# Performance work log

Hardware: AMD Instinct MI355X
Metric: run time of the kernel (lower is better)

## Reference

```python
import jax, jax.numpy as jnp
import numpy as np

N_ITEMS = 100000
H = 256
L = 3
B = 512


def setup_inputs() -> dict:
    key = jax.random.key(0)
    ks = jax.random.split(key, 9)
    s = 1.0 / np.sqrt(H)  # PyTorch GRU/Linear default uniform bound
    return {
        "input": jax.random.randint(ks[0], (B,), 0, N_ITEMS),
        "hidden": jnp.zeros((L, B, H), jnp.float32),
        "W_ih0": jax.random.uniform(ks[1], (3 * H, N_ITEMS), jnp.float32, -s, s),
        "W_ih_hi": jax.random.uniform(ks[2], (L - 1, 3 * H, H), jnp.float32, -s, s),
        "W_hh": jax.random.uniform(ks[3], (L, 3 * H, H), jnp.float32, -s, s),
        "b_ih": jax.random.uniform(ks[4], (L, 3 * H), jnp.float32, -s, s),
        "b_hh": jax.random.uniform(ks[5], (L, 3 * H), jnp.float32, -s, s),
        "W_out": jax.random.uniform(ks[6], (N_ITEMS, H), jnp.float32, -s, s),
        "b_out": jax.random.uniform(ks[7], (N_ITEMS,), jnp.float32, -s, s),
    }


def _gru_cell(x_proj, h, W_hh_l, b_hh_l):
    # PyTorch GRU cell; x_proj already holds x @ W_ih.T + b_ih
    h_proj = h @ W_hh_l.T + b_hh_l
    xr, xz, xn = jnp.split(x_proj, 3, axis=-1)
    hr, hz, hn = jnp.split(h_proj, 3, axis=-1)
    r = jax.nn.sigmoid(xr + hr)
    z = jax.nn.sigmoid(xz + hz)
    n = jnp.tanh(xn + r * hn)
    return (1.0 - z) * n + z * h


def reference(input, hidden, W_ih0, W_ih_hi, W_hh, b_ih, b_hh, W_out, b_out):
    # one_hot(input) @ W_ih0.T == row-gather of W_ih0.T  (same math, no dense one-hot)
    x_proj = W_ih0.T[input] + b_ih[0]  # (B, 3H)
    x = _gru_cell(x_proj, hidden[0], W_hh[0], b_hh[0])
    new_h = [x]
    for l in range(1, L):  # fixed small layer loop
        x_proj = x @ W_ih_hi[l - 1].T + b_ih[l]
        x = _gru_cell(x_proj, hidden[l], W_hh[l], b_hh[l])
        new_h.append(x)
    h_new = jnp.stack(new_h)  # (L, B, H)
    activation = jnp.tanh(x @ W_out.T + b_out)  # (B, N_ITEMS)
    return activation, h_new
```

## Files before the change

### kernel.cpp

```cpp
#include <hip/hip_runtime.h>
#include <math.h>
#include <stdint.h>

#define NI 100000
#define NB 512
#define NH 256
#define H3 768

typedef _Float16 f16x8 __attribute__((ext_vector_type(8)));
typedef float    f32x4 __attribute__((ext_vector_type(4)));

#define RAW_LDS_BARRIER() do {                                   \
    asm volatile("s_waitcnt lgkmcnt(0)" ::: "memory");           \
    __builtin_amdgcn_sched_barrier(0);                           \
    __builtin_amdgcn_s_barrier();                                \
    __builtin_amdgcn_sched_barrier(0);                           \
} while (0)

__device__ __forceinline__ float tanh_fast(float x) {
    x = fminf(fmaxf(x, -9.0f), 9.0f);
    const float e = __expf(2.0f * x);
    return (e - 1.0f) * __builtin_amdgcn_rcpf(e + 1.0f);
}
__device__ __forceinline__ float sigmoid_fast(float x) {
    return 1.0f / (1.0f + __expf(-x));
}

__global__ void k_gates0(const int* __restrict__ idx,
                         const float* __restrict__ Wih0,
                         const float* __restrict__ bih0,
                         const float* __restrict__ hp,
                         const float* __restrict__ hprev,
                         float* __restrict__ hnew)
{
    const int b = blockIdx.x;
    const int j = threadIdx.x;
    const int ib = idx[b];
    const float xr = Wih0[(size_t)(j          ) * NI + ib] + bih0[j];
    const float xz = Wih0[(size_t)(j + NH     ) * NI + ib] + bih0[j + NH];
    const float xn = Wih0[(size_t)(j + 2 * NH ) * NI + ib] + bih0[j + 2 * NH];
    const float hr = hp[b * H3 + j];
    const float hz = hp[b * H3 + NH + j];
    const float hn = hp[b * H3 + 2 * NH + j];
    const float h  = hprev[b * NH + j];
    const float r = sigmoid_fast(xr + hr);
    const float z = sigmoid_fast(xz + hz);
    const float n = tanh_fast(xn + r * hn);
    hnew[b * NH + j] = (1.0f - z) * n + z * h;
}

__global__ void k_gates(const float* __restrict__ xp,
                        const float* __restrict__ hp,
                        const float* __restrict__ hprev,
                        float* __restrict__ hnew)
{
    const int b = blockIdx.x;
    const int j = threadIdx.x;
    const float xr = xp[b * H3 + j];
    const float xz = xp[b * H3 + NH + j];
    const float xn = xp[b * H3 + 2 * NH + j];
    const float hr = hp[b * H3 + j];
    const float hz = hp[b * H3 + NH + j];
    const float hn = hp[b * H3 + 2 * NH + j];
    const float h  = hprev[b * NH + j];
    const float r = sigmoid_fast(xr + hr);
    const float z = sigmoid_fast(xz + hz);
    const float n = tanh_fast(xn + r * hn);
    hnew[b * NH + j] = (1.0f - z) * n + z * h;
}

__global__ void k_gates_last(const float* __restrict__ xp,
                             const float* __restrict__ hp,
                             const float* __restrict__ hprev,
                             float* __restrict__ hnew,
                             _Float16* __restrict__ Xh)
{
    const int b = blockIdx.x;
    const int j = threadIdx.x;
    const float xr = xp[b * H3 + j];
    const float xz = xp[b * H3 + NH + j];
    const float xn = xp[b * H3 + 2 * NH + j];
    const float hr = hp[b * H3 + j];
    const float hz = hp[b * H3 + NH + j];
    const float hn = hp[b * H3 + 2 * NH + j];
    const float h  = hprev[b * NH + j];
    const float r = sigmoid_fast(xr + hr);
    const float z = sigmoid_fast(xz + hz);
    const float n = tanh_fast(xn + r * hn);
    const float v = (1.0f - z) * n + z * h;
    hnew[b * NH + j] = v;
    Xh[b * NH + j] = (_Float16)v;
}

__global__ __launch_bounds__(256)
void k_gemm_small(const float* __restrict__ A0,
                  const float* __restrict__ B0,
                  const float* __restrict__ bias0,
                  float* __restrict__ C0,
                  int M, int N, int K,
                  int sA, int sB, int sBias, int sC)
{
    constexpr int BM = 64, BN = 64, BK = 64;
    __shared__ float As[BK][BM];
    __shared__ float Bs[BK][BN];

    const float* A    = A0 + (size_t)blockIdx.z * sA;
    const float* Bm   = B0 + (size_t)blockIdx.z * sB;
    const float* bias = bias0 + (size_t)blockIdx.z * sBias;
    float*       C    = C0 + (size_t)blockIdx.z * sC;

    const int tid = threadIdx.x;
    const int tx  = tid & 15;
    const int ty  = tid >> 4;
    const int m0  = blockIdx.x * BM;
    const int n0  = blockIdx.y * BN;

    float acc[4][4];
#pragma unroll
    for (int i = 0; i < 4; i++)
#pragma unroll
        for (int j = 0; j < 4; j++) acc[i][j] = 0.0f;

    for (int k0 = 0; k0 < K; k0 += BK) {
#pragma unroll
        for (int f = 0; f < 4; f++) {
            const int fid = tid + f * 256;
            const int row = fid >> 4;
            const int t4  = fid & 15;
            const int mp  = row ^ ((t4 & 3) << 3);
            {
                const float4 v = *(const float4*)(A + (size_t)(m0 + row) * K + k0 + t4 * 4);
                As[t4 * 4 + 0][mp] = v.x; As[t4 * 4 + 1][mp] = v.y;
                As[t4 * 4 + 2][mp] = v.z; As[t4 * 4 + 3][mp] = v.w;
            }
            {
                const float4 v = *(const float4*)(Bm + (size_t)(n0 + row) * K + k0 + t4 * 4);
                Bs[t4 * 4 + 0][mp] = v.x; Bs[t4 * 4 + 1][mp] = v.y;
                Bs[t4 * 4 + 2][mp] = v.z; Bs[t4 * 4 + 3][mp] = v.w;
            }
        }
        __syncthreads();
#pragma unroll
        for (int kk = 0; kk < BK; kk++) {
            const int s = ((kk >> 2) & 3) << 3;
            const float4 a0 = *(const float4*)&As[kk][(ty * 4) ^ s];
            const float4 b0 = *(const float4*)&Bs[kk][(tx * 4) ^ s];
            const float av[4] = {a0.x, a0.y, a0.z, a0.w};
            const float bv[4] = {b0.x, b0.y, b0.z, b0.w};
#pragma unroll
            for (int i = 0; i < 4; i++)
#pragma unroll
                for (int j = 0; j < 4; j++)
                    acc[i][j] = fmaf(av[i], bv[j], acc[i][j]);
        }
        __syncthreads();
    }

#pragma unroll
    for (int i = 0; i < 4; i++) {
        const size_t rowoff = (size_t)(m0 + ty * 4 + i) * N;
        const int gn = n0 + tx * 4;
        const float4 bb = *(const float4*)(bias + gn);
        float4 v;
        v.x = acc[i][0] + bb.x; v.y = acc[i][1] + bb.y;
        v.z = acc[i][2] + bb.z; v.w = acc[i][3] + bb.w;
        *(float4*)(C + rowoff + gn) = v;
    }
}

__global__ __launch_bounds__(512, 4)
void k_out_mfma(const _Float16* __restrict__ Xh,
                const float* __restrict__ W,
                const float* __restrict__ bout,
                float* __restrict__ C)
{
    __shared__ __align__(16) float S[16384];

    const int n0   = blockIdx.x * 64;
    const int tid  = threadIdx.x;
    const int w    = tid >> 6;
    const int lane = tid & 63;
    const int lr   = lane & 15;
    const int lg   = lane >> 4;

#pragma unroll
    for (int it = 0; it < 8; ++it) {
        const int fid = it * 512 + tid;
        const int row = fid >> 6;
        const int p   = fid & 63;
        int gr = n0 + row; if (gr >= NI) gr = NI - 1;
        const float* src = W + (size_t)gr * NH + (size_t)(p ^ (row & 7)) * 4;
        __builtin_amdgcn_global_load_lds(
            (const __attribute__((address_space(1))) void*)src,
            (__attribute__((address_space(3))) void*)(S + fid * 4),
            16, 0, 0);
    }

    f32x4 acc[4][4];
#pragma unroll
    for (int nf = 0; nf < 4; ++nf)
#pragma unroll
        for (int mf = 0; mf < 4; ++mf) acc[nf][mf] = (f32x4){0.f, 0.f, 0.f, 0.f};

    __syncthreads();

    const _Float16* xbase = Xh + (size_t)(w * 64 + lr) * NH + lg * 8;

#pragma unroll
    for (int t = 0; t < 8; ++t) {
        f16x8 xf[4];
#pragma unroll
        for (int mf = 0; mf < 4; ++mf)
            xf[mf] = *(const f16x8*)(xbase + mf * 16 * NH + t * 32);
#pragma unroll
        for (int nf = 0; nf < 4; ++nf) {
            const int rl = nf * 16 + lr;
            const int c0 = t * 8 + ((lg * 2)     ^ (rl & 7));
            const int c1 = t * 8 + ((lg * 2 + 1) ^ (rl & 7));
            const f32x4 u0 = *(const f32x4*)(S + rl * 256 + c0 * 4);
            const f32x4 u1 = *(const f32x4*)(S + rl * 256 + c1 * 4);
            f16x8 h;
            h[0] = (_Float16)u0[0]; h[1] = (_Float16)u0[1];
            h[2] = (_Float16)u0[2]; h[3] = (_Float16)u0[3];
            h[4] = (_Float16)u1[0]; h[5] = (_Float16)u1[1];
            h[6] = (_Float16)u1[2]; h[7] = (_Float16)u1[3];
#pragma unroll
            for (int mf = 0; mf < 4; ++mf)
                acc[nf][mf] = __builtin_amdgcn_mfma_f32_16x16x32_f16(
                    h, xf[mf], acc[nf][mf], 0, 0, 0);
        }
    }

#pragma unroll
    for (int pass = 0; pass < 2; ++pass) {
        RAW_LDS_BARRIER();
        if ((w >> 2) == pass) {
            const int mloc = (w & 3) * 64;
#pragma unroll
            for (int nf = 0; nf < 4; ++nf) {
                const int gn = n0 + nf * 16 + lg * 4;
                const float4 bb = (gn < NI) ? *(const float4*)(bout + gn)
                                            : make_float4(0.f, 0.f, 0.f, 0.f);
#pragma unroll
                for (int mf = 0; mf < 4; ++mf) {
                    const int mr = mloc + mf * 16 + lr;
                    const int p  = (nf * 4 + lg) ^ (lr & 7);
                    float4 v;
                    v.x = tanh_fast(acc[nf][mf][0] + bb.x);
                    v.y = tanh_fast(acc[nf][mf][1] + bb.y);
                    v.z = tanh_fast(acc[nf][mf][2] + bb.z);
                    v.w = tanh_fast(acc[nf][mf][3] + bb.w);
                    *(float4*)(S + mr * 64 + p * 4) = v;
                }
            }
        }
        RAW_LDS_BARRIER();
#pragma unroll
        for (int it = 0; it < 8; ++it) {
            const int fid = it * 512 + tid;
            const int row = fid >> 4;
            const int c   = fid & 15;
            const int gn  = n0 + c * 4;
            if (gn < NI) {
                const f32x4 v = *(const f32x4*)(S + row * 64 + ((c ^ (row & 7)) * 4));
                __builtin_nontemporal_store(
                    v, (f32x4*)(C + (size_t)(pass * 256 + row) * NI + gn));
            }
        }
    }
}

extern "C" void kernel_launch(void* const* d_in, const int* in_sizes, int n_in,
                              void* d_out, int out_size, void* d_ws, size_t ws_size,
                              hipStream_t stream)
{
    const int*   idx    = (const int*)  d_in[0];
    const float* hidden = (const float*)d_in[1];
    const float* Wih0   = (const float*)d_in[2];
    const float* WihHi  = (const float*)d_in[3];
    const float* Whh    = (const float*)d_in[4];
    const float* bih    = (const float*)d_in[5];
    const float* bhh    = (const float*)d_in[6];
    const float* Wout   = (const float*)d_in[7];
    const float* bout   = (const float*)d_in[8];

    float* act  = (float*)d_out;
    float* hnew = act + (size_t)NB * NI;
    float* hp = act;
    float* xp = act + 3 * NB * H3;
    _Float16* Xh = (_Float16*)d_ws;

    const dim3 bs(256);
    const dim3 gs_hp(NB / 64, H3 / 64, 3);
    const dim3 gs_xp(NB / 64, H3 / 64, 1);

    k_gemm_small<<<gs_hp, bs, 0, stream>>>(hidden, Whh, bhh, hp,
                                           NB, H3, NH, NB * NH, H3 * NH, H3, NB * H3);
    k_gates0<<<NB, bs, 0, stream>>>(idx, Wih0, bih, hp, hidden, hnew);
    k_gemm_small<<<gs_xp, bs, 0, stream>>>(hnew, WihHi, bih + H3, xp,
                                           NB, H3, NH, 0, 0, 0, 0);
    k_gates<<<NB, bs, 0, stream>>>(xp, hp + NB * H3, hidden + NB * NH, hnew + NB * NH);
    k_gemm_small<<<gs_xp, bs, 0, stream>>>(hnew + NB * NH, WihHi + H3 * NH, bih + 2 * H3, xp,
                                           NB, H3, NH, 0, 0, 0, 0);
    k_gates_last<<<NB, bs, 0, stream>>>(xp, hp + 2 * NB * H3, hidden + 2 * NB * NH,
                                        hnew + 2 * NB * NH, Xh);

    k_out_mfma<<<dim3((NI + 63) / 64), dim3(512), 0, stream>>>(Xh, Wout, bout, act);
}
```

Measured before the change: 147.3 us.

## Retile output GEMM to 128x256 blocks with double-buffered K-slice staging

The output projection kernel now tiles 128 item columns by 256 batch rows per block, with a 2x4 wave grid, instead of 64 columns by all 512 rows. W_out is staged into LDS in four 64-wide K slices, double-buffered so the next slice loads while MFMAs consume the current one. This is meant to overlap global loads with compute and cut the LDS footprint per stage. In exchange, each W_out tile is now loaded by two blocks (one per batch half), which doubles weight reads, and the loop adds extra barriers. The grid is hardcoded to 1564 blocks.

```diff
diff --git a/kernel.cpp b/kernel.cpp
--- a/kernel.cpp
+++ b/kernel.cpp
@@ -176,25 +176,33 @@
 {
     __shared__ __align__(16) float S[16384];
 
-    const int n0   = blockIdx.x * 64;
+    const int bid = blockIdx.x;
+    const int n0  = (bid >> 1) * 128;
+    const int m0  = (bid & 1) * 256;
+
     const int tid  = threadIdx.x;
     const int w    = tid >> 6;
     const int lane = tid & 63;
     const int lr   = lane & 15;
     const int lg   = lane >> 4;
-
-#pragma unroll
-    for (int it = 0; it < 8; ++it) {
-        const int fid = it * 512 + tid;
-        const int row = fid >> 6;
-        const int p   = fid & 63;
-        int gr = n0 + row; if (gr >= NI) gr = NI - 1;
-        const float* src = W + (size_t)gr * NH + (size_t)(p ^ (row & 7)) * 4;
-        __builtin_amdgcn_global_load_lds(
-            (const __attribute__((address_space(1))) void*)src,
-            (__attribute__((address_space(3))) void*)(S + fid * 4),
-            16, 0, 0);
-    }
+    const int wn   = w & 1;
+    const int wm   = w >> 1;
+
+    auto stage_q = [&](int q) {
+        float* buf = S + (q & 1) * 8192;
+#pragma unroll
+        for (int it = 0; it < 4; ++it) {
+            const int fid = it * 512 + tid;
+            const int row = fid >> 4;
+            const int p   = fid & 15;
+            int gr = n0 + row; if (gr >= NI) gr = NI - 1;
+            const float* src = W + (size_t)gr * NH + q * 64 + (size_t)(p ^ (row & 7)) * 4;
+            __builtin_amdgcn_global_load_lds(
+                (const __attribute__((address_space(1))) void*)src,
+                (__attribute__((address_space(3))) void*)(buf + fid * 4),
+                16, 0, 0);
+        }
+    };
 
     f32x4 acc[4][4];
 #pragma unroll
@@ -202,55 +210,62 @@
 #pragma unroll
         for (int mf = 0; mf < 4; ++mf) acc[nf][mf] = (f32x4){0.f, 0.f, 0.f, 0.f};
 
+    stage_q(0);
     __syncthreads();
 
-    const _Float16* xbase = Xh + (size_t)(w * 64 + lr) * NH + lg * 8;
-
-#pragma unroll
-    for (int t = 0; t < 8; ++t) {
-        f16x8 xf[4];
-#pragma unroll
-        for (int mf = 0; mf < 4; ++mf)
-            xf[mf] = *(const f16x8*)(xbase + mf * 16 * NH + t * 32);
-#pragma unroll
-        for (int nf = 0; nf < 4; ++nf) {
-            const int rl = nf * 16 + lr;
-            const int c0 = t * 8 + ((lg * 2)     ^ (rl & 7));
-            const int c1 = t * 8 + ((lg * 2 + 1) ^ (rl & 7));
-            const f32x4 u0 = *(const f32x4*)(S + rl * 256 + c0 * 4);
-            const f32x4 u1 = *(const f32x4*)(S + rl * 256 + c1 * 4);
-            f16x8 h;
-            h[0] = (_Float16)u0[0]; h[1] = (_Float16)u0[1];
-            h[2] = (_Float16)u0[2]; h[3] = (_Float16)u0[3];
-            h[4] = (_Float16)u1[0]; h[5] = (_Float16)u1[1];
-            h[6] = (_Float16)u1[2]; h[7] = (_Float16)u1[3];
+    const _Float16* xbase = Xh + (size_t)(m0 + wm * 64 + lr) * NH + lg * 8;
+
+#pragma unroll
+    for (int q = 0; q < 4; ++q) {
+        if (q < 3) stage_q(q + 1);
+        const float* buf = S + (q & 1) * 8192;
+#pragma unroll
+        for (int tt = 0; tt < 2; ++tt) {
+            f16x8 xf[4];
 #pragma unroll
             for (int mf = 0; mf < 4; ++mf)
-                acc[nf][mf] = __builtin_amdgcn_mfma_f32_16x16x32_f16(
-                    h, xf[mf], acc[nf][mf], 0, 0, 0);
-        }
+                xf[mf] = *(const f16x8*)(xbase + mf * 16 * NH + q * 64 + tt * 32);
+#pragma unroll
+            for (int nf = 0; nf < 4; ++nf) {
+                const int rl = wn * 64 + nf * 16 + lr;
+                const int c0 = (tt * 8 + lg * 2)     ^ (rl & 7);
+                const int c1 = (tt * 8 + lg * 2 + 1) ^ (rl & 7);
+                const f32x4 u0 = *(const f32x4*)(buf + rl * 64 + c0 * 4);
+                const f32x4 u1 = *(const f32x4*)(buf + rl * 64 + c1 * 4);
+                f16x8 h;
+                h[0] = (_Float16)u0[0]; h[1] = (_Float16)u0[1];
+                h[2] = (_Float16)u0[2]; h[3] = (_Float16)u0[3];
+                h[4] = (_Float16)u1[0]; h[5] = (_Float16)u1[1];
+                h[6] = (_Float16)u1[2]; h[7] = (_Float16)u1[3];
+#pragma unroll
+                for (int mf = 0; mf < 4; ++mf)
+                    acc[nf][mf] = __builtin_amdgcn_mfma_f32_16x16x32_f16(
+                        h, xf[mf], acc[nf][mf], 0, 0, 0);
+            }
+        }
+        if (q < 3) __syncthreads();
     }
 
 #pragma unroll
     for (int pass = 0; pass < 2; ++pass) {
         RAW_LDS_BARRIER();
-        if ((w >> 2) == pass) {
-            const int mloc = (w & 3) * 64;
+        if ((wm >> 1) == pass) {
 #pragma unroll
             for (int nf = 0; nf < 4; ++nf) {
-                const int gn = n0 + nf * 16 + lg * 4;
+                const int gn = n0 + wn * 64 + nf * 16 + lg * 4;
                 const float4 bb = (gn < NI) ? *(const float4*)(bout + gn)
                                             : make_float4(0.f, 0.f, 0.f, 0.f);
+                const int q4 = wn * 16 + nf * 4 + lg;
 #pragma unroll
                 for (int mf = 0; mf < 4; ++mf) {
-                    const int mr = mloc + mf * 16 + lr;
-                    const int p  = (nf * 4 + lg) ^ (lr & 7);
+                    const int mr   = (wm & 1) * 64 + mf * 16 + lr;
+                    const int slot = q4 ^ (lr & 7);
                     float4 v;
                     v.x = tanh_fast(acc[nf][mf][0] + bb.x);
                     v.y = tanh_fast(acc[nf][mf][1] + bb.y);
                     v.z = tanh_fast(acc[nf][mf][2] + bb.z);
                     v.w = tanh_fast(acc[nf][mf][3] + bb.w);
-                    *(float4*)(S + mr * 64 + p * 4) = v;
+                    *(float4*)(S + mr * 128 + slot * 4) = v;
                 }
             }
         }
@@ -258,13 +273,13 @@
 #pragma unroll
         for (int it = 0; it < 8; ++it) {
             const int fid = it * 512 + tid;
-            const int row = fid >> 4;
-            const int c   = fid & 15;
+            const int row = fid >> 5;
+            const int c   = fid & 31;
             const int gn  = n0 + c * 4;
             if (gn < NI) {
-                const f32x4 v = *(const f32x4*)(S + row * 64 + ((c ^ (row & 7)) * 4));
+                const f32x4 v = *(const f32x4*)(S + row * 128 + ((c ^ (row & 7)) * 4));
                 __builtin_nontemporal_store(
-                    v, (f32x4*)(C + (size_t)(pass * 256 + row) * NI + gn));
+                    v, (f32x4*)(C + (size_t)(m0 + pass * 128 + row) * NI + gn));
             }
         }
     }
@@ -305,5 +320,5 @@
     k_gates_last<<<NB, bs, 0, stream>>>(xp, hp + 2 * NB * H3, hidden + 2 * NB * NH,
                                         hnew + 2 * NB * NH, Xh);
 
-    k_out_mfma<<<dim3((NI + 63) / 64), dim3(512), 0, stream>>>(Xh, Wout, bout, act);
-}
+    k_out_mfma<<<dim3(1564), dim3(512), 0, stream>>>(Xh, Wout, bout, act);
+}
```

After: 161.1 us. +9.3%, slower.
